# Kernel optimization log

Measured on AMD Instinct MI355X. Metric: run time of the kernel, lower is better.

Reference implementation:

```python
import jax, jax.numpy as jnp
import numpy as np

B, C, D, H, W = 2, 128, 32, 64, 64  # ch_in=128, shurink=0 -> Cs = ch_out = C
Cs = C


def setup_inputs() -> dict:
    key = jax.random.key(0)
    ks = jax.random.split(key, 9)
    std = 1.0 / np.sqrt(C).astype(np.float32)
    x = jax.random.normal(ks[0], (B, C, D, H, W), jnp.float32)
    Wk = jax.random.normal(ks[1], (Cs, C), jnp.float32) * std
    bk = jax.random.normal(ks[2], (Cs,), jnp.float32) * std
    Wq = jax.random.normal(ks[3], (Cs, C), jnp.float32) * std
    bq = jax.random.normal(ks[4], (Cs,), jnp.float32) * std
    Wv = jax.random.normal(ks[5], (Cs, C), jnp.float32) * std
    bv = jax.random.normal(ks[6], (Cs,), jnp.float32) * std
    Wo = jax.random.normal(ks[7], (C, Cs), jnp.float32) * (1.0 / np.sqrt(Cs).astype(np.float32))
    bo = jax.random.normal(ks[8], (C,), jnp.float32) * std
    return {"x": x, "Wk": Wk, "bk": bk, "Wq": Wq, "bq": bq, "Wv": Wv, "bv": bv, "Wo": Wo, "bo": bo}


def reference(x, Wk, bk, Wq, bq, Wv, bv, Wo, bo):
    # 1x1x1 Conv3d == per-voxel linear over channels
    def proj(Wt, bt):
        return jnp.einsum('bcdhw,oc->bodhw', x, Wt) + bt[None, :, None, None, None]

    K = proj(Wk, bk)  # [B,Cs,D,H,W]
    Q = proj(Wq, bq)
    V = proj(Wv, bv)

    scale = 1.0 / jnp.sqrt(jnp.asarray(Cs, x.dtype))
    # per-pixel depth attention: scores[b,h,w,i,j] = sum_c K[b,c,i,h,w] * Q[b,c,j,h,w]
    scores = jnp.einsum('bcihw,bcjhw->bhwij', K, Q) * scale
    # torch softmax dim=1 on [N,D,D] == key-position axis i (axis=-2 here)
    A = jax.nn.softmax(scores, axis=-2)
    # a[b,c,j,h,w] = sum_i V[b,c,i,h,w] * A[b,h,w,i,j]  (== bmm(V, A))
    a = jnp.einsum('bcihw,bhwij->bcjhw', V, A)
    out = jnp.einsum('bcjhw,oc->bojhw', a, Wo) + bo[None, :, None, None, None]
    return x + out  # atten_factor = 1
```

## Files before the change

kernel.cpp:

```cpp
#include <hip/hip_runtime.h>

typedef _Float16 f16x8 __attribute__((ext_vector_type(8)));
typedef _Float16 f16x4 __attribute__((ext_vector_type(4)));
typedef float    f32x4 __attribute__((ext_vector_type(4)));

#define MFMA(a,b,c) __builtin_amdgcn_mfma_f32_16x16x32_f16((a),(b),(c),0,0,0)


__global__ __launch_bounds__(128) void prep_kernel(
    const float* __restrict__ Wk, const float* __restrict__ bk,
    const float* __restrict__ Wq, const float* __restrict__ bq,
    const float* __restrict__ Wv, const float* __restrict__ bv,
    const float* __restrict__ Wo, const float* __restrict__ bo,
    _Float16* __restrict__ wh, float* __restrict__ bf) {
  __shared__ float shK[128], shO[128];
  const int o = blockIdx.x;
  const int c = threadIdx.x;
  const float scale = 0.08838834764831844f;
  shK[c] = Wk[c*128 + o];
  shO[c] = Wo[o*128 + c];
  __syncthreads();
  float aM = 0.f, aV = 0.f, tK = 0.f, bV = 0.f;
  for (int m = 0; m < 128; ++m) {
    aM += shK[m] * Wq[m*128 + c];
    aV += shO[m] * Wv[m*128 + c];
    tK += shK[m] * bq[m];
    bV += shO[m] * bv[m];
  }
  wh[o*128 + c]         = (_Float16)(aM * scale);
  wh[16384 + o*128 + c] = (_Float16)aV;
  if (c == 0) { bf[o] = tK * scale; bf[128 + o] = bV + bo[o]; }
}

__global__ __launch_bounds__(256) void transpose_kernel(
    const float* __restrict__ x, _Float16* __restrict__ Xg) {
  __shared__ _Float16 Lt[64 * 132];
  const int bid = blockIdx.x;
  const int h = bid & 63, d = (bid >> 6) & 31, b = bid >> 11;
  const int tid = threadIdx.x;
  const int wq = tid & 15, cr = tid >> 4;
  const size_t rbase = (size_t)b*16777216u + (size_t)d*4096 + h*64;
#pragma unroll
  for (int pass = 0; pass < 2; ++pass) {
    const int base_c = pass*64 + cr*4;
    f32x4 v[4];
#pragma unroll
    for (int r = 0; r < 4; ++r)
      v[r] = *(const f32x4*)(x + rbase + (size_t)(base_c + r)*131072 + wq*4);
#pragma unroll
    for (int p = 0; p < 4; ++p) {
      f16x4 t;
#pragma unroll
      for (int r = 0; r < 4; ++r) t[r] = (_Float16)v[r][p];
      *(f16x4*)(Lt + (wq*4 + p)*132 + base_c) = t;
    }
  }
  __syncthreads();
  const int gbase = b*1024 + h*16;
#pragma unroll
  for (int i = 0; i < 4; ++i) {
    const int idx = tid + i*256;
    const int w = idx >> 4, ck = (idx & 15) * 8;
    const f16x8 v = *(const f16x8*)(Lt + w*132 + ck);
    *(f16x8*)(Xg + (size_t)(gbase + (w>>2))*16384 + (d*4 + (w&3))*128 + ck) = v;
  }
}

__device__ __forceinline__ f16x4 cvt4(f32x4 v, f32x4 b) {
  f16x4 r;
  r[0] = (_Float16)(v[0] + b[0]); r[1] = (_Float16)(v[1] + b[1]);
  r[2] = (_Float16)(v[2] + b[2]); r[3] = (_Float16)(v[3] + b[3]);
  return r;
}
__device__ __forceinline__ f16x4 cvt4z(f32x4 v) {
  f16x4 r;
  r[0] = (_Float16)v[0]; r[1] = (_Float16)v[1];
  r[2] = (_Float16)v[2]; r[3] = (_Float16)v[3];
  return r;
}

__device__ __forceinline__ int xsw(int row, int col ) {
  return ((row << 8) | (col << 1)) ^ (((row ^ (row >> 2)) & 7) << 4);
}

__global__ __launch_bounds__(1024, 8) void attn_kernel(
    const _Float16* __restrict__ Xg, const _Float16* __restrict__ wh,
    const float* __restrict__ bfp, float* __restrict__ out) {
  __shared__ __align__(16) char lds[75776];
  char* XtB = lds;
  char* YtB = lds + 32768;
  _Float16* At = (_Float16*)(lds + 65536);

  const int tid  = threadIdx.x;
  const int lane = tid & 63;
  const int wv   = tid >> 6;
  const int quad = lane >> 4;
  const int l15  = lane & 15;

  const int bid = blockIdx.x;
  const int g = (bid & ~31) | ((bid & 7) << 2) | ((bid >> 3) & 3);
  const int b   = g >> 10;
  const int rem = g & 1023;
  const int h   = rem >> 4;
  const int wg  = rem & 15;
  const size_t pbase = (size_t)b * 16777216u + (size_t)(h*64 + wg*4);
  const f32x4 zz = {0.f, 0.f, 0.f, 0.f};

  const int mi = wv & 7, ni = wv >> 3;
  f16x8 wm[4];
#pragma unroll
  for (int kk = 0; kk < 4; ++kk)
    wm[kk] = *(const f16x8*)(wh + (mi*16 + l15)*128 + kk*32 + quad*8);
  const f32x4 t4 = *(const f32x4*)(bfp + mi*16 + quad*4);

  {
    const _Float16* src = Xg + (size_t)g * 16384;
#pragma unroll
    for (int i = 0; i < 2; ++i) {
      const int idx = tid + i*1024;
      const int row = idx >> 4, ck = (idx & 15) * 8;
      const f16x8 v = *(const f16x8*)(src + row*128 + ck);
      *(f16x8*)(XtB + xsw(row, ck)) = v;
    }
  }
  __syncthreads();

  {
    f32x4 aY[4] = {zz, zz, zz, zz};
#pragma unroll
    for (int kk = 0; kk < 4; ++kk) {
      const int co = kk*32 + quad*8;
#pragma unroll
      for (int nt = 0; nt < 4; ++nt) {
        const f16x8 bfv = *(const f16x8*)(XtB + xsw(ni*64 + nt*16 + l15, co));
        aY[nt] = MFMA(wm[kk], bfv, aY[nt]);
      }
    }
#pragma unroll
    for (int nt = 0; nt < 4; ++nt)
      *(f16x4*)(YtB + xsw(ni*64 + nt*16 + l15, mi*16 + quad*4)) = cvt4(aY[nt], t4);
  }
  __syncthreads();

  if (wv < 4) {
    const int p = wv;
    f32x4 aS[2][2] = {{zz, zz}, {zz, zz}};
#pragma unroll
    for (int kk = 0; kk < 4; ++kk) {
      const int co = kk*32 + quad*8;
      f16x8 ak[2], by[2];
#pragma unroll
      for (int t = 0; t < 2; ++t) {
        ak[t] = *(const f16x8*)(XtB + xsw((t*16 + l15)*4 + p, co));
        by[t] = *(const f16x8*)(YtB + xsw((t*16 + l15)*4 + p, co));
      }
#pragma unroll
      for (int ti = 0; ti < 2; ++ti)
#pragma unroll
        for (int tj = 0; tj < 2; ++tj)
          aS[ti][tj] = MFMA(ak[ti], by[tj], aS[ti][tj]);
    }
#pragma unroll
    for (int tj = 0; tj < 2; ++tj) {
      float mx = aS[0][tj][0];
#pragma unroll
      for (int r = 1; r < 4; ++r) mx = fmaxf(mx, aS[0][tj][r]);
#pragma unroll
      for (int r = 0; r < 4; ++r) mx = fmaxf(mx, aS[1][tj][r]);
      mx = fmaxf(mx, __shfl_xor(mx, 16));
      mx = fmaxf(mx, __shfl_xor(mx, 32));
      float e[2][4];
      float den = 0.f;
#pragma unroll
      for (int ti = 0; ti < 2; ++ti)
#pragma unroll
        for (int r = 0; r < 4; ++r) { e[ti][r] = __expf(aS[ti][tj][r] - mx); den += e[ti][r]; }
      den += __shfl_xor(den, 16);
      den += __shfl_xor(den, 32);
      const float rr = 1.0f / den;
#pragma unroll
      for (int ti = 0; ti < 2; ++ti) {
        f16x4 av;
#pragma unroll
        for (int r = 0; r < 4; ++r) av[r] = (_Float16)(e[ti][r] * rr);
        *(f16x4*)(At + (p*32 + tj*16 + l15)*40 + ti*16 + quad*4) = av;
      }
    }
  }
  __syncthreads();

  f16x8 wp[4];
  {
#pragma unroll
    for (int kk = 0; kk < 4; ++kk)
      wp[kk] = *(const f16x8*)(wh + 16384 + ((wv & 7)*16 + l15)*128 + kk*32 + quad*8);
    const int p = wv & 3, mg = wv >> 2;
    f16x8 bA[2];
#pragma unroll
    for (int tj = 0; tj < 2; ++tj)
      bA[tj] = *(const f16x8*)(At + (p*32 + tj*16 + l15)*40 + quad*8);
#pragma unroll
    for (int t2 = 0; t2 < 2; ++t2) {
      const int ms = mg*2 + t2;
      f16x8 ax;
#pragma unroll
      for (int jj = 0; jj < 8; ++jj)
        ax[jj] = *(const _Float16*)(XtB + xsw((quad*8 + jj)*4 + p, ms*16 + l15));
#pragma unroll
      for (int tj = 0; tj < 2; ++tj) {
        const f32x4 aU = MFMA(ax, bA[tj], zz);
        *(f16x4*)(YtB + xsw((tj*16 + l15)*4 + p, ms*16 + quad*4)) = cvt4z(aU);
      }
    }
  }
  __syncthreads();

  {
    const int oi = wv & 7, mg6 = wv >> 3;
    f32x4 acc[4] = {zz, zz, zz, zz};
#pragma unroll
    for (int kk = 0; kk < 4; ++kk) {
      const int co = kk*32 + quad*8;
#pragma unroll
      for (int mt = 0; mt < 4; ++mt) {
        const f16x8 av = *(const f16x8*)(YtB + xsw((mg6*4 + mt)*16 + l15, co));
        acc[mt] = MFMA(av, wp[kk], acc[mt]);
      }
    }
    const int o = oi*16 + l15;
    const float bb = bfp[128 + o];
    float* outp = out + pbase + (size_t)o*131072;
#pragma unroll
    for (int mt = 0; mt < 4; ++mt) {
      const int colb = (mg6*4 + mt)*16 + quad*4;
      const int d = colb >> 2;
      f32x4 v;
#pragma unroll
      for (int r = 0; r < 4; ++r)
        v[r] = acc[mt][r] + bb +
               (float)*(const _Float16*)(XtB + xsw(colb + r, o));
      *(f32x4*)(outp + (size_t)d*4096) = v;
    }
  }
}

extern "C" void kernel_launch(void* const* d_in, const int* in_sizes, int n_in,
                              void* d_out, int out_size, void* d_ws, size_t ws_size,
                              hipStream_t stream) {
  const float* x  = (const float*)d_in[0];
  const float* Wk = (const float*)d_in[1];
  const float* bk = (const float*)d_in[2];
  const float* Wq = (const float*)d_in[3];
  const float* bq = (const float*)d_in[4];
  const float* Wv = (const float*)d_in[5];
  const float* bv = (const float*)d_in[6];
  const float* Wo = (const float*)d_in[7];
  const float* bo = (const float*)d_in[8];
  float* out = (float*)d_out;
  _Float16* wh = (_Float16*)d_ws;
  float* bf = (float*)((char*)d_ws + 65536);
  _Float16* Xg = (_Float16*)((char*)d_ws + 131072);

  prep_kernel<<<dim3(128), dim3(128), 0, stream>>>(Wk, bk, Wq, bq, Wv, bv, Wo, bo, wh, bf);
  transpose_kernel<<<dim3(4096), dim3(256), 0, stream>>>(x, Xg);
  attn_kernel<<<dim3(2048), dim3(1024), 0, stream>>>(Xg, wh, bf, out);
}
```

Baseline: 364.6 us.

## Process eight pixels per attention block instead of four

Each attention workgroup now handles 8 w-positions (256 voxel rows) instead of 4. The LDS footprint doubles to about 148KB, the grid halves to 1024 blocks, and the score/softmax stage now keeps all 16 waves busy instead of only 4. The transpose output layout, the swizzle function and the block-index remap are adjusted to match. This amortizes the per-block weight loads and the idle waves in the softmax stage, at the cost of lower occupancy: only one block fits per CU given the LDS size.

```diff
diff --git a/kernel.cpp b/kernel.cpp
--- a/kernel.cpp
+++ b/kernel.cpp
@@ -56,13 +56,13 @@
     }
   }
   __syncthreads();
-  const int gbase = b*1024 + h*16;
+  const int gbase = (b*64 + h)*8;
 #pragma unroll
   for (int i = 0; i < 4; ++i) {
     const int idx = tid + i*256;
     const int w = idx >> 4, ck = (idx & 15) * 8;
     const f16x8 v = *(const f16x8*)(Lt + w*132 + ck);
-    *(f16x8*)(Xg + (size_t)(gbase + (w>>2))*16384 + (d*4 + (w&3))*128 + ck) = v;
+    *(f16x8*)(Xg + (size_t)(gbase + (w>>3))*32768 + (d*8 + (w&7))*128 + ck) = v;
   }
 }
 
@@ -80,16 +80,16 @@
 }
 
 __device__ __forceinline__ int xsw(int row, int col ) {
-  return ((row << 8) | (col << 1)) ^ (((row ^ (row >> 2)) & 7) << 4);
-}
-
-__global__ __launch_bounds__(1024, 8) void attn_kernel(
+  return ((row << 8) | (col << 1)) ^ (((row ^ (row >> 3) ^ (row >> 5)) & 7) << 4);
+}
+
+__global__ __launch_bounds__(1024, 4) void attn_kernel(
     const _Float16* __restrict__ Xg, const _Float16* __restrict__ wh,
     const float* __restrict__ bfp, float* __restrict__ out) {
-  __shared__ __align__(16) char lds[75776];
+  __shared__ __align__(16) char lds[151552];
   char* XtB = lds;
-  char* YtB = lds + 32768;
-  _Float16* At = (_Float16*)(lds + 65536);
+  char* YtB = lds + 65536;
+  _Float16* At = (_Float16*)(lds + 131072);
 
   const int tid  = threadIdx.x;
   const int lane = tid & 63;
@@ -98,12 +98,12 @@
   const int l15  = lane & 15;
 
   const int bid = blockIdx.x;
-  const int g = (bid & ~31) | ((bid & 7) << 2) | ((bid >> 3) & 3);
-  const int b   = g >> 10;
-  const int rem = g & 1023;
-  const int h   = rem >> 4;
-  const int wg  = rem & 15;
-  const size_t pbase = (size_t)b * 16777216u + (size_t)(h*64 + wg*4);
+  const int g = (bid & ~15) | ((bid & 7) << 1) | ((bid >> 3) & 1);
+  const int b   = g >> 9;
+  const int rem = g & 511;
+  const int h   = rem >> 3;
+  const int wg  = rem & 7;
+  const size_t pbase = (size_t)b * 16777216u + (size_t)(h*64 + wg*8);
   const f32x4 zz = {0.f, 0.f, 0.f, 0.f};
 
   const int mi = wv & 7, ni = wv >> 3;
@@ -114,9 +114,9 @@
   const f32x4 t4 = *(const f32x4*)(bfp + mi*16 + quad*4);
 
   {
-    const _Float16* src = Xg + (size_t)g * 16384;
-#pragma unroll
-    for (int i = 0; i < 2; ++i) {
+    const _Float16* src = Xg + (size_t)g * 32768;
+#pragma unroll
+    for (int i = 0; i < 4; ++i) {
       const int idx = tid + i*1024;
       const int row = idx >> 4, ck = (idx & 15) * 8;
       const f16x8 v = *(const f16x8*)(src + row*128 + ck);
@@ -126,65 +126,57 @@
   __syncthreads();
 
   {
-    f32x4 aY[4] = {zz, zz, zz, zz};
+    f32x4 aY[8] = {zz, zz, zz, zz, zz, zz, zz, zz};
 #pragma unroll
     for (int kk = 0; kk < 4; ++kk) {
       const int co = kk*32 + quad*8;
 #pragma unroll
-      for (int nt = 0; nt < 4; ++nt) {
-        const f16x8 bfv = *(const f16x8*)(XtB + xsw(ni*64 + nt*16 + l15, co));
+      for (int nt = 0; nt < 8; ++nt) {
+        const f16x8 bfv = *(const f16x8*)(XtB + xsw(ni*128 + nt*16 + l15, co));
         aY[nt] = MFMA(wm[kk], bfv, aY[nt]);
       }
     }
 #pragma unroll
-    for (int nt = 0; nt < 4; ++nt)
-      *(f16x4*)(YtB + xsw(ni*64 + nt*16 + l15, mi*16 + quad*4)) = cvt4(aY[nt], t4);
-  }
-  __syncthreads();
-
-  if (wv < 4) {
-    const int p = wv;
-    f32x4 aS[2][2] = {{zz, zz}, {zz, zz}};
+    for (int nt = 0; nt < 8; ++nt)
+      *(f16x4*)(YtB + xsw(ni*128 + nt*16 + l15, mi*16 + quad*4)) = cvt4(aY[nt], t4);
+  }
+  __syncthreads();
+
+  {
+    const int p = wv & 7, tj = wv >> 3;
+    f32x4 aS[2] = {zz, zz};
 #pragma unroll
     for (int kk = 0; kk < 4; ++kk) {
       const int co = kk*32 + quad*8;
-      f16x8 ak[2], by[2];
-#pragma unroll
-      for (int t = 0; t < 2; ++t) {
-        ak[t] = *(const f16x8*)(XtB + xsw((t*16 + l15)*4 + p, co));
-        by[t] = *(const f16x8*)(YtB + xsw((t*16 + l15)*4 + p, co));
-      }
-#pragma unroll
-      for (int ti = 0; ti < 2; ++ti)
-#pragma unroll
-        for (int tj = 0; tj < 2; ++tj)
-          aS[ti][tj] = MFMA(ak[ti], by[tj], aS[ti][tj]);
-    }
-#pragma unroll
-    for (int tj = 0; tj < 2; ++tj) {
-      float mx = aS[0][tj][0];
-#pragma unroll
-      for (int r = 1; r < 4; ++r) mx = fmaxf(mx, aS[0][tj][r]);
-#pragma unroll
-      for (int r = 0; r < 4; ++r) mx = fmaxf(mx, aS[1][tj][r]);
-      mx = fmaxf(mx, __shfl_xor(mx, 16));
-      mx = fmaxf(mx, __shfl_xor(mx, 32));
-      float e[2][4];
-      float den = 0.f;
-#pragma unroll
-      for (int ti = 0; ti < 2; ++ti)
-#pragma unroll
-        for (int r = 0; r < 4; ++r) { e[ti][r] = __expf(aS[ti][tj][r] - mx); den += e[ti][r]; }
-      den += __shfl_xor(den, 16);
-      den += __shfl_xor(den, 32);
-      const float rr = 1.0f / den;
+      const f16x8 by = *(const f16x8*)(YtB + xsw((tj*16 + l15)*8 + p, co));
 #pragma unroll
       for (int ti = 0; ti < 2; ++ti) {
-        f16x4 av;
-#pragma unroll
-        for (int r = 0; r < 4; ++r) av[r] = (_Float16)(e[ti][r] * rr);
-        *(f16x4*)(At + (p*32 + tj*16 + l15)*40 + ti*16 + quad*4) = av;
-      }
+        const f16x8 ak = *(const f16x8*)(XtB + xsw((ti*16 + l15)*8 + p, co));
+        aS[ti] = MFMA(ak, by, aS[ti]);
+      }
+    }
+    float mx = aS[0][0];
+#pragma unroll
+    for (int r = 1; r < 4; ++r) mx = fmaxf(mx, aS[0][r]);
+#pragma unroll
+    for (int r = 0; r < 4; ++r) mx = fmaxf(mx, aS[1][r]);
+    mx = fmaxf(mx, __shfl_xor(mx, 16));
+    mx = fmaxf(mx, __shfl_xor(mx, 32));
+    float e[2][4];
+    float den = 0.f;
+#pragma unroll
+    for (int ti = 0; ti < 2; ++ti)
+#pragma unroll
+      for (int r = 0; r < 4; ++r) { e[ti][r] = __expf(aS[ti][r] - mx); den += e[ti][r]; }
+    den += __shfl_xor(den, 16);
+    den += __shfl_xor(den, 32);
+    const float rr = 1.0f / den;
+#pragma unroll
+    for (int ti = 0; ti < 2; ++ti) {
+      f16x4 av;
+#pragma unroll
+      for (int r = 0; r < 4; ++r) av[r] = (_Float16)(e[ti][r] * rr);
+      *(f16x4*)(At + (p*32 + tj*16 + l15)*40 + ti*16 + quad*4) = av;
     }
   }
   __syncthreads();
@@ -193,23 +185,23 @@
   {
 #pragma unroll
     for (int kk = 0; kk < 4; ++kk)
-      wp[kk] = *(const f16x8*)(wh + 16384 + ((wv & 7)*16 + l15)*128 + kk*32 + quad*8);
-    const int p = wv & 3, mg = wv >> 2;
+      wp[kk] = *(const f16x8*)(wh + 16384 + (mi*16 + l15)*128 + kk*32 + quad*8);
+    const int p = wv & 7, mg = wv >> 3;
     f16x8 bA[2];
 #pragma unroll
     for (int tj = 0; tj < 2; ++tj)
       bA[tj] = *(const f16x8*)(At + (p*32 + tj*16 + l15)*40 + quad*8);
 #pragma unroll
-    for (int t2 = 0; t2 < 2; ++t2) {
-      const int ms = mg*2 + t2;
+    for (int t2 = 0; t2 < 4; ++t2) {
+      const int ms = mg*4 + t2;
       f16x8 ax;
 #pragma unroll
       for (int jj = 0; jj < 8; ++jj)
-        ax[jj] = *(const _Float16*)(XtB + xsw((quad*8 + jj)*4 + p, ms*16 + l15));
+        ax[jj] = *(const _Float16*)(XtB + xsw((quad*8 + jj)*8 + p, ms*16 + l15));
 #pragma unroll
       for (int tj = 0; tj < 2; ++tj) {
         const f32x4 aU = MFMA(ax, bA[tj], zz);
-        *(f16x4*)(YtB + xsw((tj*16 + l15)*4 + p, ms*16 + quad*4)) = cvt4z(aU);
+        *(f16x4*)(YtB + xsw((tj*16 + l15)*8 + p, ms*16 + quad*4)) = cvt4z(aU);
       }
     }
   }
@@ -217,13 +209,13 @@
 
   {
     const int oi = wv & 7, mg6 = wv >> 3;
-    f32x4 acc[4] = {zz, zz, zz, zz};
+    f32x4 acc[8] = {zz, zz, zz, zz, zz, zz, zz, zz};
 #pragma unroll
     for (int kk = 0; kk < 4; ++kk) {
       const int co = kk*32 + quad*8;
 #pragma unroll
-      for (int mt = 0; mt < 4; ++mt) {
-        const f16x8 av = *(const f16x8*)(YtB + xsw((mg6*4 + mt)*16 + l15, co));
+      for (int mt = 0; mt < 8; ++mt) {
+        const f16x8 av = *(const f16x8*)(YtB + xsw((mg6*8 + mt)*16 + l15, co));
         acc[mt] = MFMA(av, wp[kk], acc[mt]);
       }
     }
@@ -231,15 +223,15 @@
     const float bb = bfp[128 + o];
     float* outp = out + pbase + (size_t)o*131072;
 #pragma unroll
-    for (int mt = 0; mt < 4; ++mt) {
-      const int colb = (mg6*4 + mt)*16 + quad*4;
-      const int d = colb >> 2;
+    for (int mt = 0; mt < 8; ++mt) {
+      const int vox0 = (mg6*8 + mt)*16 + quad*4;
+      const int d = vox0 >> 3;
       f32x4 v;
 #pragma unroll
       for (int r = 0; r < 4; ++r)
         v[r] = acc[mt][r] + bb +
-               (float)*(const _Float16*)(XtB + xsw(colb + r, o));
-      *(f32x4*)(outp + (size_t)d*4096) = v;
+               (float)*(const _Float16*)(XtB + xsw(vox0 + r, o));
+      *(f32x4*)(outp + (size_t)d*4096 + (vox0 & 7)) = v;
     }
   }
 }
@@ -263,5 +255,5 @@
 
   prep_kernel<<<dim3(128), dim3(128), 0, stream>>>(Wk, bk, Wq, bq, Wv, bv, Wo, bo, wh, bf);
   transpose_kernel<<<dim3(4096), dim3(256), 0, stream>>>(x, Xg);
-  attn_kernel<<<dim3(2048), dim3(1024), 0, stream>>>(Xg, wh, bf, out);
-}
+  attn_kernel<<<dim3(1024), dim3(1024), 0, stream>>>(Xg, wh, bf, out);
+}
```

After: 343.6 us. 5.8% less time.
